# Optimization experiments

Hardware: AMD Instinct MI355X
Metric: run time of the kernel (lower is better)

The kernel has to match this reference:

```python
import jax, jax.numpy as jnp
import numpy as np

N = 100000
E = 1600000
IN_FEATS = 128
H_FEATS = 64
BN_EPS = 1e-5


def setup_inputs() -> dict:
    key = jax.random.key(0)
    ks = jax.random.split(key, 8)
    features = jax.random.normal(ks[0], (N, IN_FEATS), dtype=jnp.float32)
    src = jax.random.randint(ks[1], (E,), 0, N, dtype=jnp.int32)
    dst = jax.random.randint(ks[2], (E,), 0, N, dtype=jnp.int32)
    # GraphConv weights (Glorot-ish scale) and biases
    W1 = jax.random.normal(ks[3], (IN_FEATS, H_FEATS), dtype=jnp.float32) / np.sqrt(IN_FEATS)
    b1 = jnp.zeros((H_FEATS,), dtype=jnp.float32)
    W2 = jax.random.normal(ks[4], (H_FEATS, H_FEATS), dtype=jnp.float32) / np.sqrt(H_FEATS)
    b2 = jnp.zeros((H_FEATS,), dtype=jnp.float32)
    gamma1 = jnp.ones((H_FEATS,), dtype=jnp.float32)
    beta1 = jnp.zeros((H_FEATS,), dtype=jnp.float32)
    gamma2 = jnp.ones((H_FEATS,), dtype=jnp.float32)
    beta2 = jnp.zeros((H_FEATS,), dtype=jnp.float32)
    return {"features": features, "W1": W1, "b1": b1, "gamma1": gamma1,
            "beta1": beta1, "W2": W2, "b2": b2, "gamma2": gamma2,
            "beta2": beta2, "src": src, "dst": dst}


def _degrees(src, dst):
    ones = jnp.ones((E,), dtype=jnp.float32)
    deg_out = jax.ops.segment_sum(ones, src, num_segments=N)
    deg_in = jax.ops.segment_sum(ones, dst, num_segments=N)
    # DGL clamps degree to >= 1 to avoid div by zero
    norm_src = jax.lax.rsqrt(jnp.maximum(deg_out, 1.0))  # [N]
    norm_dst = jax.lax.rsqrt(jnp.maximum(deg_in, 1.0))   # [N]
    return norm_src, norm_dst


def _graph_conv(x, W, b, src, dst, norm_src, norm_dst):
    # norm='both': D_out^{-1/2} scaling on src, sum-aggregate, D_in^{-1/2} on dst
    h = x * norm_src[:, None]          # [N, in]
    h = h @ W                          # [N, out] (transform before aggregate)
    msgs = h[src]                      # [E, out] gather
    agg = jax.ops.segment_sum(msgs, dst, num_segments=N)  # [N, out] scatter-add
    out = agg * norm_dst[:, None] + b
    return jax.nn.elu(out)


def _batch_norm(x, gamma, beta):
    mean = jnp.mean(x, axis=0)
    var = jnp.mean(jnp.square(x - mean), axis=0)
    return (x - mean) * jax.lax.rsqrt(var + BN_EPS) * gamma + beta


def reference(features, W1, b1, gamma1, beta1, W2, b2, gamma2, beta2, src, dst):
    # dropout p=0.0 (eval) -> identity
    norm_src, norm_dst = _degrees(src, dst)
    h1 = _graph_conv(features, W1, b1, src, dst, norm_src, norm_dst)
    h1 = _batch_norm(h1, gamma1, beta1)
    h2 = _graph_conv(h1, W2, b2, src, dst, norm_src, norm_dst)
    h2 = _batch_norm(h2, gamma2, beta2)
    return h2
```

## Files before the change

kernel.cpp:

```cpp
#include <hip/hip_runtime.h>
#include <cmath>

#define NFEAT_IN 128
#define NFEAT_H 64
#define BN_EPS 1e-5f
#define SCAP 2560
#define EPB 4096
#define NBMAX 800

typedef unsigned short ushort_t;
typedef unsigned int uint_t;
typedef __attribute__((ext_vector_type(8))) short short8v;
typedef __attribute__((ext_vector_type(4))) float f32x4;

__device__ inline float b2f(ushort_t u) {
    return __uint_as_float(((uint_t)u) << 16);
}

__device__ inline ushort_t f2b(float f) {
    uint_t x = __float_as_uint(f);
    return (ushort_t)((x + 0x7FFFu + ((x >> 16) & 1u)) >> 16);
}


__global__ __launch_bounds__(256) void block_append_kernel(const int* __restrict__ src,
                                                           const int* __restrict__ dst,
                                                           int* __restrict__ deg_s,
                                                           int* __restrict__ curD,
                                                           uint_t* __restrict__ dbuf,
                                                           int E, int NB) {
    __shared__ int lcnt[NBMAX];
    __shared__ int lcur[NBMAX];
    int t = threadIdx.x;
    int e0 = blockIdx.x * EPB;
    int e1 = min(e0 + EPB, E);
    for (int i = t; i < NB; i += 256) lcnt[i] = 0;
    __syncthreads();
    for (int e = e0 + t; e < e1; e += 256)
        atomicAdd(&lcnt[dst[e] >> 7], 1);
    __syncthreads();
    for (int i = t; i < NB; i += 256) {
        int c = lcnt[i];
        lcur[i] = (c > 0) ? atomicAdd(&curD[i * 16], c) : 0;
    }
    __syncthreads();
    for (int e = e0 + t; e < e1; e += 256) {
        int s = src[e], d = dst[e];
        atomicAdd(&deg_s[s], 1);
        int pos = atomicAdd(&lcur[d >> 7], 1);
        if (pos < SCAP) dbuf[(long long)(d >> 7) * SCAP + pos] = ((uint_t)s << 7) | (uint_t)(d & 127);
    }
}

__global__ __launch_bounds__(256) void deg_append_kernel(const int* __restrict__ src,
                                                         const int* __restrict__ dst,
                                                         int* __restrict__ deg_s,
                                                         int* __restrict__ curD,
                                                         uint_t* __restrict__ dbuf, int E) {
    int e = blockIdx.x * 256 + threadIdx.x;
    if (e < E) {
        int s = src[e], d = dst[e];
        atomicAdd(&deg_s[s], 1);
        int pD = atomicAdd(&curD[(d >> 7) * 16], 1);
        if (pD < SCAP) dbuf[(long long)(d >> 7) * SCAP + pD] = ((uint_t)s << 7) | (uint_t)(d & 127);
    }
}

__global__ __launch_bounds__(256) void bucket_hist_kernel(const uint_t* __restrict__ dbuf,
                                                          const int* __restrict__ curD,
                                                          int* __restrict__ deg_d, int N) {
    __shared__ int hist[128];
    int bb = blockIdx.x;
    int t = threadIdx.x;
    if (t < 128) hist[t] = 0;
    __syncthreads();
    int cnt = curD[bb * 16];
    if (cnt > SCAP) cnt = SCAP;
    long long base = (long long)bb * SCAP;
    for (int i = t; i < cnt; i += 256) atomicAdd(&hist[dbuf[base + i] & 127], 1);
    __syncthreads();
    if (t < 128) {
        int node = bb * 128 + t;
        if (node < N) deg_d[node] = hist[t];
    }
}

__global__ __launch_bounds__(256) void norm_scan_kernel(const int* __restrict__ deg_s,
                                                        const int* __restrict__ deg_d,
                                                        float* __restrict__ norm_s,
                                                        float* __restrict__ norm_d,
                                                        int* __restrict__ start,
                                                        int* __restrict__ counter,
                                                        float* __restrict__ stats, int N) {
    int tid = threadIdx.x;
    int i = blockIdx.x * 256 + tid;
    if (blockIdx.x == 0 && tid < 128) stats[tid] = 0.f;
    int lane = tid & 63, w = tid >> 6;
    int ds = 0, dd = 0;
    if (i < N) { ds = deg_s[i]; dd = deg_d[i]; }
    int pd = (dd + 7) & ~7;

    int x = pd;
#pragma unroll
    for (int off = 1; off < 64; off <<= 1) {
        int y = __shfl_up(x, off, 64);
        if (lane >= off) x += y;
    }
    __shared__ int wsum[4];
    __shared__ int blockbase;
    if (lane == 63) wsum[w] = x;
    __syncthreads();
    if (tid == 0)
        blockbase = atomicAdd(counter, wsum[0] + wsum[1] + wsum[2] + wsum[3]);
    __syncthreads();
    int base = blockbase;
    for (int ww = 0; ww < w; ++ww) base += wsum[ww];
    int st = base + x - pd;

    if (i < N) {
        norm_s[i] = rsqrtf((float)(ds > 1 ? ds : 1));
        norm_d[i] = rsqrtf((float)(dd > 1 ? dd : 1));
        start[i] = st;
    }
}

__global__ __launch_bounds__(256) void bucket_scatter_kernel(const uint_t* __restrict__ dbuf,
                                                             const int* __restrict__ curD,
                                                             const int* __restrict__ start,
                                                             int* __restrict__ col, int N) {
    __shared__ int cur[128];
    __shared__ int sst[128];
    int b = blockIdx.x, t = threadIdx.x;
    if (t < 128) {
        cur[t] = 0;
        int node = b * 128 + t;
        sst[t] = (node < N) ? start[node] : 0;
    }
    __syncthreads();
    int cnt = curD[b * 16];
    if (cnt > SCAP) cnt = SCAP;
    long long base = (long long)b * SCAP;
    for (int i = t; i < cnt; i += 256) {
        uint_t p = dbuf[base + i];
        int d0 = (int)(p & 127u);
        int s = (int)(p >> 7);
        int off = atomicAdd(&cur[d0], 1);
        col[sst[d0] + off] = s;
    }
}


__global__ __launch_bounds__(256) void gemm1_mfma(const float* __restrict__ x,
                                                  const float* __restrict__ W,
                                                  const float* __restrict__ norm,
                                                  ushort_t* __restrict__ out, int n) {
    constexpr int K = 128;
    __shared__ ushort_t sWh[64 * K];
    __shared__ ushort_t sWl[64 * K];
    int tid = threadIdx.x;
    for (int i = tid; i < K * 64; i += 256) {
        int k = i >> 6, f = i & 63;
        float v = W[i];
        ushort_t hi = f2b(v);
        ushort_t lo = f2b(v - b2f(hi));
        int idx = f * K + (((k >> 3) ^ (f & 7)) << 3) + (k & 7);
        sWh[idx] = hi;
        sWl[idx] = lo;
    }
    int w = tid >> 6, l = tid & 63, g = l >> 4;
    int rA = blockIdx.x * 64 + w * 16 + (l & 15);
    f32x4 acc[4];
#pragma unroll
    for (int nt = 0; nt < 4; ++nt) acc[nt] = (f32x4){0.f, 0.f, 0.f, 0.f};
    __syncthreads();

#pragma unroll
    for (int ks = 0; ks < K / 32; ++ks) {
        float av[8];
        if (rA < n) {
            const float* px = x + (long long)rA * K + ks * 32 + g * 8;
            float4 p0 = *(const float4*)px;
            float4 p1 = *(const float4*)(px + 4);
            av[0] = p0.x; av[1] = p0.y; av[2] = p0.z; av[3] = p0.w;
            av[4] = p1.x; av[5] = p1.y; av[6] = p1.z; av[7] = p1.w;
        } else {
#pragma unroll
            for (int j = 0; j < 8; ++j) av[j] = 0.f;
        }
        short8v ah, al;
#pragma unroll
        for (int j = 0; j < 8; ++j) {
            ushort_t h = f2b(av[j]);
            ah[j] = (short)h;
            al[j] = (short)f2b(av[j] - b2f(h));
        }
#pragma unroll
        for (int nt = 0; nt < 4; ++nt) {
            int f = nt * 16 + (l & 15);
            int c = (ks * 4 + g) ^ (f & 7);
            short8v bh = *(const short8v*)&sWh[f * K + (c << 3)];
            short8v bl = *(const short8v*)&sWl[f * K + (c << 3)];
            acc[nt] = __builtin_amdgcn_mfma_f32_16x16x32_bf16(ah, bh, acc[nt], 0, 0, 0);
            acc[nt] = __builtin_amdgcn_mfma_f32_16x16x32_bf16(ah, bl, acc[nt], 0, 0, 0);
            acc[nt] = __builtin_amdgcn_mfma_f32_16x16x32_bf16(al, bh, acc[nt], 0, 0, 0);
        }
    }
    int rb = blockIdx.x * 64 + w * 16 + g * 4;
    float nv[4];
#pragma unroll
    for (int j = 0; j < 4; ++j) {
        int r = rb + j;
        nv[j] = (r < n) ? norm[r] : 0.f;
    }
#pragma unroll
    for (int nt = 0; nt < 4; ++nt) {
        int cc = nt * 16 + (l & 15);
#pragma unroll
        for (int j = 0; j < 4; ++j) {
            int r = rb + j;
            if (r < n) out[(long long)r * 64 + cc] = f2b(acc[nt][j] * nv[j]);
        }
    }
}

__global__ __launch_bounds__(256) void gemm2_mfma(const ushort_t* __restrict__ x,
                                                  const float* __restrict__ W,
                                                  const float* __restrict__ coef,
                                                  const float* __restrict__ biasK,
                                                  const float* __restrict__ norm,
                                                  ushort_t* __restrict__ out, int n) {
    constexpr int K = 64;
    __shared__ ushort_t sWh[64 * K];
    __shared__ ushort_t sWl[64 * K];
    int tid = threadIdx.x;
    for (int i = tid; i < K * 64; i += 256) {
        int k = i >> 6, f = i & 63;
        float v = coef[k] * W[i];
        ushort_t hi = f2b(v);
        ushort_t lo = f2b(v - b2f(hi));
        int idx = f * K + (((k >> 3) ^ (f & 7)) << 3) + (k & 7);
        sWh[idx] = hi;
        sWl[idx] = lo;
    }
    int w = tid >> 6, l = tid & 63, g = l >> 4;
    int rA = blockIdx.x * 64 + w * 16 + (l & 15);
    f32x4 acc[4];
#pragma unroll
    for (int nt = 0; nt < 4; ++nt) acc[nt] = (f32x4){0.f, 0.f, 0.f, 0.f};
    __syncthreads();

#pragma unroll
    for (int ks = 0; ks < 2; ++ks) {
        short8v ah;
        if (rA < n) {
            uint4 u = *(const uint4*)(x + (long long)rA * 64 + ks * 32 + g * 8);
            union { uint4 u; short8v s; } cvt;
            cvt.u = u;
            ah = cvt.s;
        } else {
#pragma unroll
            for (int j = 0; j < 8; ++j) ah[j] = 0;
        }
#pragma unroll
        for (int nt = 0; nt < 4; ++nt) {
            int f = nt * 16 + (l & 15);
            int c = (ks * 4 + g) ^ (f & 7);
            short8v bh = *(const short8v*)&sWh[f * K + (c << 3)];
            short8v bl = *(const short8v*)&sWl[f * K + (c << 3)];
            acc[nt] = __builtin_amdgcn_mfma_f32_16x16x32_bf16(ah, bh, acc[nt], 0, 0, 0);
            acc[nt] = __builtin_amdgcn_mfma_f32_16x16x32_bf16(ah, bl, acc[nt], 0, 0, 0);
        }
    }
    int rb = blockIdx.x * 64 + w * 16 + g * 4;
    float nv[4];
#pragma unroll
    for (int j = 0; j < 4; ++j) {
        int r = rb + j;
        nv[j] = (r < n) ? norm[r] : 0.f;
    }
#pragma unroll
    for (int nt = 0; nt < 4; ++nt) {
        int cc = nt * 16 + (l & 15);
        float bk = biasK[cc];
#pragma unroll
        for (int j = 0; j < 4; ++j) {
            int r = rb + j;
            if (r < n) out[(long long)r * 64 + cc] = f2b((acc[nt][j] + bk) * nv[j]);
        }
    }
}

__global__ __launch_bounds__(256) void agg_fused_kernel(const ushort_t* __restrict__ h,
                                                        const int* __restrict__ start,
                                                        const int* __restrict__ degd,
                                                        const int* __restrict__ col,
                                                        const float* __restrict__ normd,
                                                        const float* __restrict__ bias,
                                                        ushort_t* __restrict__ outp,
                                                        float* __restrict__ stats, int N) {
    int tid = threadIdx.x;
    int w = tid >> 6;
    int lane = tid & 63;
    int g = lane >> 3;
    int j = lane & 7;

    float bb[8];
#pragma unroll
    for (int i = 0; i < 8; ++i) bb[i] = bias[j * 8 + i];

    float sum[8], sq[8];
#pragma unroll
    for (int i = 0; i < 8; ++i) { sum[i] = 0.f; sq[i] = 0.f; }

    for (int node = blockIdx.x * 4 + w; node < N; node += gridDim.x * 4) {
        int s0 = start[node];
        int d = degd[node];
        float acc[8];
#pragma unroll
        for (int i = 0; i < 8; ++i) acc[i] = 0.f;

        int k = 0;
        for (; k + 16 <= d; k += 16) {
            int c0 = col[s0 + k + g];
            int c1 = col[s0 + k + 8 + g];
            uint4 a = ((const uint4*)(h + (long long)c0 * 64))[j];
            uint4 b = ((const uint4*)(h + (long long)c1 * 64))[j];
            acc[0] += __uint_as_float(a.x << 16);
            acc[1] += __uint_as_float(a.x & 0xFFFF0000u);
            acc[2] += __uint_as_float(a.y << 16);
            acc[3] += __uint_as_float(a.y & 0xFFFF0000u);
            acc[4] += __uint_as_float(a.z << 16);
            acc[5] += __uint_as_float(a.z & 0xFFFF0000u);
            acc[6] += __uint_as_float(a.w << 16);
            acc[7] += __uint_as_float(a.w & 0xFFFF0000u);
            acc[0] += __uint_as_float(b.x << 16);
            acc[1] += __uint_as_float(b.x & 0xFFFF0000u);
            acc[2] += __uint_as_float(b.y << 16);
            acc[3] += __uint_as_float(b.y & 0xFFFF0000u);
            acc[4] += __uint_as_float(b.z << 16);
            acc[5] += __uint_as_float(b.z & 0xFFFF0000u);
            acc[6] += __uint_as_float(b.w << 16);
            acc[7] += __uint_as_float(b.w & 0xFFFF0000u);
        }
        for (; k + 8 <= d; k += 8) {
            int c0 = col[s0 + k + g];
            uint4 a = ((const uint4*)(h + (long long)c0 * 64))[j];
            acc[0] += __uint_as_float(a.x << 16);
            acc[1] += __uint_as_float(a.x & 0xFFFF0000u);
            acc[2] += __uint_as_float(a.y << 16);
            acc[3] += __uint_as_float(a.y & 0xFFFF0000u);
            acc[4] += __uint_as_float(a.z << 16);
            acc[5] += __uint_as_float(a.z & 0xFFFF0000u);
            acc[6] += __uint_as_float(a.w << 16);
            acc[7] += __uint_as_float(a.w & 0xFFFF0000u);
        }
        if (k < d) {
            int idx = k + g;
            if (idx < d) {
                int c0 = col[s0 + idx];
                uint4 a = ((const uint4*)(h + (long long)c0 * 64))[j];
                acc[0] += __uint_as_float(a.x << 16);
                acc[1] += __uint_as_float(a.x & 0xFFFF0000u);
                acc[2] += __uint_as_float(a.y << 16);
                acc[3] += __uint_as_float(a.y & 0xFFFF0000u);
                acc[4] += __uint_as_float(a.z << 16);
                acc[5] += __uint_as_float(a.z & 0xFFFF0000u);
                acc[6] += __uint_as_float(a.w << 16);
                acc[7] += __uint_as_float(a.w & 0xFFFF0000u);
            }
        }

#pragma unroll
        for (int i = 0; i < 8; ++i) {
            acc[i] += __shfl_xor(acc[i], 8, 64);
            acc[i] += __shfl_xor(acc[i], 16, 64);
            acc[i] += __shfl_xor(acc[i], 32, 64);
        }

        if (g == 0) {
            float nv = normd[node];
            float v[8];
#pragma unroll
            for (int i = 0; i < 8; ++i) {
                float t = acc[i] * nv + bb[i];
                t = t > 0.f ? t : expm1f(t);
                v[i] = t;
                sum[i] += t;
                sq[i] += t * t;
            }
            uint4 p;
            p.x = ((uint_t)f2b(v[1]) << 16) | f2b(v[0]);
            p.y = ((uint_t)f2b(v[3]) << 16) | f2b(v[2]);
            p.z = ((uint_t)f2b(v[5]) << 16) | f2b(v[4]);
            p.w = ((uint_t)f2b(v[7]) << 16) | f2b(v[6]);
            ((uint4*)(outp + (long long)node * 64))[j] = p;
        }
    }

    __shared__ float ssum[4][64];
    __shared__ float ssq[4][64];
    if (g == 0) {
#pragma unroll
        for (int i = 0; i < 8; ++i) {
            ssum[w][j * 8 + i] = sum[i];
            ssq[w][j * 8 + i] = sq[i];
        }
    }
    __syncthreads();
    if (tid < 64) {
        float s = ssum[0][tid] + ssum[1][tid] + ssum[2][tid] + ssum[3][tid];
        float q = ssq[0][tid] + ssq[1][tid] + ssq[2][tid] + ssq[3][tid];
        atomicAdd(&stats[tid], s);
        atomicAdd(&stats[64 + tid], q);
    }
}

__global__ __launch_bounds__(64) void bn_fin2_kernel(float* __restrict__ stats,
                                                     const float* __restrict__ gamma,
                                                     const float* __restrict__ beta,
                                                     const float* __restrict__ W2,
                                                     float* __restrict__ coef,
                                                     float* __restrict__ biasK, float inv_n) {
    int f = threadIdx.x;
    float mean = stats[f] * inv_n;
    float var = stats[64 + f] * inv_n - mean * mean;
    float a = gamma[f] * rsqrtf(var + BN_EPS);
    float cB = beta[f] - mean * a;
    coef[f] = a;
    coef[64 + f] = cB;
    stats[f] = 0.f;
    stats[64 + f] = 0.f;
    __shared__ float scB[64];
    scB[f] = cB;
    __syncthreads();
    float s = 0.f;
    for (int k = 0; k < 64; ++k) s = fmaf(scB[k], W2[k * 64 + f], s);
    biasK[f] = s;
}

__global__ __launch_bounds__(64) void bn_finalize(float* __restrict__ stats,
                                                  const float* __restrict__ gamma,
                                                  const float* __restrict__ beta,
                                                  float* __restrict__ coef, float inv_n) {
    int f = threadIdx.x;
    float mean = stats[f] * inv_n;
    float var = stats[64 + f] * inv_n - mean * mean;
    float a = gamma[f] * rsqrtf(var + BN_EPS);
    coef[f] = a;
    coef[64 + f] = beta[f] - mean * a;
}

__global__ __launch_bounds__(256) void bn_apply_b2f(const uint4* __restrict__ in,
                                                    const float* __restrict__ coef,
                                                    float4* __restrict__ out, long long n4) {
    long long i = (long long)blockIdx.x * 256 + threadIdx.x;
    if (i >= n4) return;
    int k = (int)((i & 7) << 3);
    uint4 u = in[i];
    float4 a, b;
    a.x = __uint_as_float(u.x << 16) * coef[k] + coef[64 + k];
    a.y = __uint_as_float(u.x & 0xFFFF0000u) * coef[k + 1] + coef[64 + k + 1];
    a.z = __uint_as_float(u.y << 16) * coef[k + 2] + coef[64 + k + 2];
    a.w = __uint_as_float(u.y & 0xFFFF0000u) * coef[k + 3] + coef[64 + k + 3];
    b.x = __uint_as_float(u.z << 16) * coef[k + 4] + coef[64 + k + 4];
    b.y = __uint_as_float(u.z & 0xFFFF0000u) * coef[k + 5] + coef[64 + k + 5];
    b.z = __uint_as_float(u.w << 16) * coef[k + 6] + coef[64 + k + 6];
    b.w = __uint_as_float(u.w & 0xFFFF0000u) * coef[k + 7] + coef[64 + k + 7];
    out[i * 2] = a;
    out[i * 2 + 1] = b;
}


extern "C" void kernel_launch(void* const* d_in, const int* in_sizes, int n_in,
                              void* d_out, int out_size, void* d_ws, size_t ws_size,
                              hipStream_t stream) {
    const float* features = (const float*)d_in[0];
    const float* W1 = (const float*)d_in[1];
    const float* b1 = (const float*)d_in[2];
    const float* gamma1 = (const float*)d_in[3];
    const float* beta1 = (const float*)d_in[4];
    const float* W2 = (const float*)d_in[5];
    const float* b2 = (const float*)d_in[6];
    const float* gamma2 = (const float*)d_in[7];
    const float* beta2 = (const float*)d_in[8];
    const int* src = (const int*)d_in[9];
    const int* dst = (const int*)d_in[10];
    int N = in_sizes[0] / NFEAT_IN;
    int E = in_sizes[9];

    float inv_n = 1.0f / (float)N;
    long long tot = (long long)N * 64;
    int eblk256 = (E + 255) / 256;
    int nblk256 = (N + 255) / 256;
    int NB = (N + 127) >> 7;
    int gblk = (N + 63) / 64;
    long long n4 = (long long)N * 8;
    int a4blk = (int)((n4 + 255) / 256);

    long long bufcap = (long long)NB * SCAP;
    long long colcap = (long long)E + 8LL * N;
    long long int_total = (16LL * NB + 4 + 3LL * N + bufcap + colcap + 3) & ~3LL;
    long long flt_count = ((2LL * N + 128 + 128 + 64) + 3) & ~3LL;

    int* ip = (int*)d_ws;
    int* curD = ip;
    int* counter = ip + 16LL * NB;
    int* deg_s = ip + 16LL * NB + 4;
    int* deg_d = deg_s + N;
    int* startv = deg_d + N;
    uint_t* dbuf = (uint_t*)(startv + N);
    int* col = (int*)(dbuf + bufcap);
    float* fp = (float*)(ip + int_total);
    float* norm_s = fp;
    float* norm_d = fp + N;
    float* stats = fp + 2LL * N;
    float* coef = stats + 128;
    float* biasK = coef + 128;
    ushort_t* hA = (ushort_t*)(fp + flt_count);
    ushort_t* oB = hA + tot;

    hipMemsetAsync(curD, 0, sizeof(int) * (16LL * NB + 4 + N), stream);
    if (NB <= NBMAX) {
        int bblk = (E + EPB - 1) / EPB;
        block_append_kernel<<<bblk, 256, 0, stream>>>(src, dst, deg_s, curD, dbuf, E, NB);
    } else {
        deg_append_kernel<<<eblk256, 256, 0, stream>>>(src, dst, deg_s, curD, dbuf, E);
    }
    bucket_hist_kernel<<<NB, 256, 0, stream>>>(dbuf, curD, deg_d, N);
    norm_scan_kernel<<<nblk256, 256, 0, stream>>>(deg_s, deg_d, norm_s, norm_d,
                                                  startv, counter, stats, N);
    bucket_scatter_kernel<<<NB, 256, 0, stream>>>(dbuf, curD, startv, col, N);

    gemm1_mfma<<<gblk, 256, 0, stream>>>(features, W1, norm_s, hA, N);
    agg_fused_kernel<<<2048, 256, 0, stream>>>(hA, startv, deg_d, col, norm_d, b1,
                                               oB, stats, N);
    bn_fin2_kernel<<<1, 64, 0, stream>>>(stats, gamma1, beta1, W2, coef, biasK, inv_n);

    gemm2_mfma<<<gblk, 256, 0, stream>>>(oB, W2, coef, biasK, norm_s, hA, N);
    agg_fused_kernel<<<2048, 256, 0, stream>>>(hA, startv, deg_d, col, norm_d, b2,
                                               oB, stats, N);
    bn_finalize<<<1, 64, 0, stream>>>(stats, gamma2, beta2, coef, inv_n);
    bn_apply_b2f<<<a4blk, 256, 0, stream>>>((const uint4*)oB, coef, (float4*)d_out, n4);
}
```

Baseline: 416.6 us.

## Quantize node features to int8 with per-row scale before gather-aggregate

```diff
diff --git a/kernel.cpp b/kernel.cpp
--- a/kernel.cpp
+++ b/kernel.cpp
@@ -5,7 +5,7 @@
 #define NFEAT_H 64
 #define BN_EPS 1e-5f
 #define SCAP 2560
-#define EPB 4096
+#define EPB 8192
 #define NBMAX 800
 
 typedef unsigned short ushort_t;
@@ -290,7 +290,56 @@
     }
 }
 
-__global__ __launch_bounds__(256) void agg_fused_kernel(const ushort_t* __restrict__ h,
+__global__ __launch_bounds__(256) void quant8_kernel(const ushort_t* __restrict__ h,
+                                                     uint2* __restrict__ q8,
+                                                     float* __restrict__ qs, int N) {
+    int tid = threadIdx.x;
+    int w = tid >> 6, lane = tid & 63;
+    int j = lane & 7;
+    int row = blockIdx.x * 32 + w * 8 + (lane >> 3);
+    if (row >= N) return;
+    uint4 u = ((const uint4*)(h + (long long)row * 64))[j];
+    float v[8];
+    v[0] = __uint_as_float(u.x << 16);
+    v[1] = __uint_as_float(u.x & 0xFFFF0000u);
+    v[2] = __uint_as_float(u.y << 16);
+    v[3] = __uint_as_float(u.y & 0xFFFF0000u);
+    v[4] = __uint_as_float(u.z << 16);
+    v[5] = __uint_as_float(u.z & 0xFFFF0000u);
+    v[6] = __uint_as_float(u.w << 16);
+    v[7] = __uint_as_float(u.w & 0xFFFF0000u);
+    float m = 0.f;
+#pragma unroll
+    for (int i = 0; i < 8; ++i) m = fmaxf(m, fabsf(v[i]));
+    m = fmaxf(m, __shfl_xor(m, 1, 64));
+    m = fmaxf(m, __shfl_xor(m, 2, 64));
+    m = fmaxf(m, __shfl_xor(m, 4, 64));
+    float inv = (m > 0.f) ? 127.f / m : 0.f;
+    if (j == 0) qs[row] = (m > 0.f) ? m * (1.f / 127.f) : 0.f;
+    int q[8];
+#pragma unroll
+    for (int i = 0; i < 8; ++i) q[i] = __float2int_rn(v[i] * inv);
+    uint2 p;
+    p.x = (uint_t)(q[0] & 255) | ((uint_t)(q[1] & 255) << 8) |
+          ((uint_t)(q[2] & 255) << 16) | ((uint_t)q[3] << 24);
+    p.y = (uint_t)(q[4] & 255) | ((uint_t)(q[5] & 255) << 8) |
+          ((uint_t)(q[6] & 255) << 16) | ((uint_t)q[7] << 24);
+    q8[(long long)row * 8 + j] = p;
+}
+
+__device__ inline void acc_i8(float* acc, uint2 u, float sc) {
+    acc[0] += sc * (float)(int)(signed char)(u.x);
+    acc[1] += sc * (float)(int)(signed char)(u.x >> 8);
+    acc[2] += sc * (float)(int)(signed char)(u.x >> 16);
+    acc[3] += sc * (float)(int)(signed char)(u.x >> 24);
+    acc[4] += sc * (float)(int)(signed char)(u.y);
+    acc[5] += sc * (float)(int)(signed char)(u.y >> 8);
+    acc[6] += sc * (float)(int)(signed char)(u.y >> 16);
+    acc[7] += sc * (float)(int)(signed char)(u.y >> 24);
+}
+
+__global__ __launch_bounds__(256) void agg_fused_kernel(const uint2* __restrict__ q8,
+                                                        const float* __restrict__ qs,
                                                         const int* __restrict__ start,
                                                         const int* __restrict__ degd,
                                                         const int* __restrict__ col,
@@ -323,50 +372,26 @@
         for (; k + 16 <= d; k += 16) {
             int c0 = col[s0 + k + g];
             int c1 = col[s0 + k + 8 + g];
-            uint4 a = ((const uint4*)(h + (long long)c0 * 64))[j];
-            uint4 b = ((const uint4*)(h + (long long)c1 * 64))[j];
-            acc[0] += __uint_as_float(a.x << 16);
-            acc[1] += __uint_as_float(a.x & 0xFFFF0000u);
-            acc[2] += __uint_as_float(a.y << 16);
-            acc[3] += __uint_as_float(a.y & 0xFFFF0000u);
-            acc[4] += __uint_as_float(a.z << 16);
-            acc[5] += __uint_as_float(a.z & 0xFFFF0000u);
-            acc[6] += __uint_as_float(a.w << 16);
-            acc[7] += __uint_as_float(a.w & 0xFFFF0000u);
-            acc[0] += __uint_as_float(b.x << 16);
-            acc[1] += __uint_as_float(b.x & 0xFFFF0000u);
-            acc[2] += __uint_as_float(b.y << 16);
-            acc[3] += __uint_as_float(b.y & 0xFFFF0000u);
-            acc[4] += __uint_as_float(b.z << 16);
-            acc[5] += __uint_as_float(b.z & 0xFFFF0000u);
-            acc[6] += __uint_as_float(b.w << 16);
-            acc[7] += __uint_as_float(b.w & 0xFFFF0000u);
+            uint2 a = q8[(long long)c0 * 8 + j];
+            uint2 b = q8[(long long)c1 * 8 + j];
+            float sa = qs[c0];
+            float sb = qs[c1];
+            acc_i8(acc, a, sa);
+            acc_i8(acc, b, sb);
         }
         for (; k + 8 <= d; k += 8) {
             int c0 = col[s0 + k + g];
-            uint4 a = ((const uint4*)(h + (long long)c0 * 64))[j];
-            acc[0] += __uint_as_float(a.x << 16);
-            acc[1] += __uint_as_float(a.x & 0xFFFF0000u);
-            acc[2] += __uint_as_float(a.y << 16);
-            acc[3] += __uint_as_float(a.y & 0xFFFF0000u);
-            acc[4] += __uint_as_float(a.z << 16);
-            acc[5] += __uint_as_float(a.z & 0xFFFF0000u);
-            acc[6] += __uint_as_float(a.w << 16);
-            acc[7] += __uint_as_float(a.w & 0xFFFF0000u);
+            uint2 a = q8[(long long)c0 * 8 + j];
+            float sa = qs[c0];
+            acc_i8(acc, a, sa);
         }
         if (k < d) {
             int idx = k + g;
             if (idx < d) {
                 int c0 = col[s0 + idx];
-                uint4 a = ((const uint4*)(h + (long long)c0 * 64))[j];
-                acc[0] += __uint_as_float(a.x << 16);
-                acc[1] += __uint_as_float(a.x & 0xFFFF0000u);
-                acc[2] += __uint_as_float(a.y << 16);
-                acc[3] += __uint_as_float(a.y & 0xFFFF0000u);
-                acc[4] += __uint_as_float(a.z << 16);
-                acc[5] += __uint_as_float(a.z & 0xFFFF0000u);
-                acc[6] += __uint_as_float(a.w << 16);
-                acc[7] += __uint_as_float(a.w & 0xFFFF0000u);
+                uint2 a = q8[(long long)c0 * 8 + j];
+                float sa = qs[c0];
+                acc_i8(acc, a, sa);
             }
         }
 
@@ -494,6 +519,7 @@
     int nblk256 = (N + 255) / 256;
     int NB = (N + 127) >> 7;
     int gblk = (N + 63) / 64;
+    int qblk = (N + 31) / 32;
     long long n4 = (long long)N * 8;
     int a4blk = (int)((n4 + 255) / 256);
 
@@ -518,6 +544,8 @@
     float* biasK = coef + 128;
     ushort_t* hA = (ushort_t*)(fp + flt_count);
     ushort_t* oB = hA + tot;
+    float* qs = (float*)(oB + tot);
+    uint2* q8 = (uint2*)(qs + N);
 
     hipMemsetAsync(curD, 0, sizeof(int) * (16LL * NB + 4 + N), stream);
     if (NB <= NBMAX) {
@@ -532,12 +560,14 @@
     bucket_scatter_kernel<<<NB, 256, 0, stream>>>(dbuf, curD, startv, col, N);
 
     gemm1_mfma<<<gblk, 256, 0, stream>>>(features, W1, norm_s, hA, N);
-    agg_fused_kernel<<<2048, 256, 0, stream>>>(hA, startv, deg_d, col, norm_d, b1,
+    quant8_kernel<<<qblk, 256, 0, stream>>>(hA, q8, qs, N);
+    agg_fused_kernel<<<2048, 256, 0, stream>>>(q8, qs, startv, deg_d, col, norm_d, b1,
                                                oB, stats, N);
     bn_fin2_kernel<<<1, 64, 0, stream>>>(stats, gamma1, beta1, W2, coef, biasK, inv_n);
 
     gemm2_mfma<<<gblk, 256, 0, stream>>>(oB, W2, coef, biasK, norm_s, hA, N);
-    agg_fused_kernel<<<2048, 256, 0, stream>>>(hA, startv, deg_d, col, norm_d, b2,
+    quant8_kernel<<<qblk, 256, 0, stream>>>(hA, q8, qs, N);
+    agg_fused_kernel<<<2048, 256, 0, stream>>>(q8, qs, startv, deg_d, col, norm_d, b2,
                                                oB, stats, N);
     bn_finalize<<<1, 64, 0, stream>>>(stats, gamma2, beta2, coef, inv_n);
     bn_apply_b2f<<<a4blk, 256, 0, stream>>>((const uint4*)oB, coef, (float4*)d_out, n4);
```

Result: faster. 404.1 us (-3.0%).
